# Kernel optimization log

Hardware: AMD Instinct MI355X
Metric: run time of the kernel (lower is better)

Reference implementation:

```python
import jax, jax.numpy as jnp
import numpy as np

EMBED_DIM = 1024
B, T = 8, 2048


def setup_inputs() -> dict:
    key = jax.random.key(0)
    kx, kw, kb = jax.random.split(key, 3)
    x = jax.random.normal(kx, (B, T, EMBED_DIM), dtype=jnp.float32)
    # nn.Linear(embed_dim, 3*embed_dim): weight [3E, E], bias [3E]
    bound = 1.0 / np.sqrt(EMBED_DIM)
    W = jax.random.uniform(kw, (3 * EMBED_DIM, EMBED_DIM), minval=-bound, maxval=bound, dtype=jnp.float32)
    b = jax.random.uniform(kb, (3 * EMBED_DIM,), minval=-bound, maxval=bound, dtype=jnp.float32)
    return {"x": x, "W": W, "b": b}


def reference(x, W, b):
    E = x.shape[-1]
    qkv = jnp.einsum('bte,fe->btf', x, W) + b            # [B,T,3E]
    q, k, v = jnp.split(qkv, 3, axis=-1)                 # each [B,T,E]
    scale = 1.0 / jnp.sqrt(jnp.asarray(E, dtype=x.dtype))
    scores = jnp.einsum('bqe,bke->bqk', q, k) * scale    # [B,T,T]
    Tq = x.shape[1]
    causal = jnp.tril(jnp.ones((Tq, Tq), dtype=bool))
    scores = jnp.where(causal[None, :, :], scores, jnp.asarray(-jnp.inf, dtype=x.dtype))
    attn = jax.nn.softmax(scores, axis=-1)
    y = jnp.einsum('bqk,bke->bqe', attn, v)              # [B,T,E]
    return y
```

## Files before the change

kernel.cpp:

```cpp
#include <hip/hip_runtime.h>

typedef unsigned short u16;
typedef unsigned int u32;
typedef __attribute__((ext_vector_type(4))) float f32x4;
typedef __attribute__((ext_vector_type(8))) short bf16x8;

#define T_DIM 2048
#define E_DIM 1024
#define NBATCH 8
#define BK 32
#define BUF 32768
#define CORE_LDS (3 * BUF)

struct alignas(8)  U16x4 { u16 x, y, z, w; };
struct alignas(16) F32x4 { float x, y, z, w; };

__device__ __forceinline__ u16 f2bf(float f) {
  u32 u = __float_as_uint(f);
  u += 0x7FFFu + ((u >> 16) & 1u);
  return (u16)(u >> 16);
}

__device__ __forceinline__ void gld16(u16* lds, const u16* g) {
  __builtin_amdgcn_global_load_lds((const __attribute__((address_space(1))) void*)g,
                                   (__attribute__((address_space(3))) void*)lds, 16, 0, 0);
}

__device__ __forceinline__ u32 swz7(u32 x) { return x ^ (((x >> 7) & 7u) << 4); }

__device__ __forceinline__ int xcd_swz(int orig, int nwg) {
  int q = nwg >> 3, r = nwg & 7;
  int x = orig & 7, l = orig >> 3;
  return (x < r ? x * (q + 1) : r * (q + 1) + (x - r) * q) + l;
}

#define LGKM0_PIN() do { asm volatile("s_waitcnt lgkmcnt(0)" ::: "memory"); \
                         __builtin_amdgcn_sched_barrier(0); } while (0)

template <typename HOOK>
__device__ __forceinline__ void gemm256(const u16* __restrict__ A, const u16* __restrict__ B,
                                        int lda, int ldb, int nK, char* lds0, f32x4 acc[8][4],
                                        HOOK&& hook)
{
  const int tid = threadIdx.x, lane = tid & 63, wave = tid >> 6;
  const int wr = wave >> 2, wc = wave & 3;

  const u16* sAp[2]; const u16* sBp[2];
#pragma unroll
  for (int c = 0; c < 2; ++c) {
    u32 L = (u32)(c * 8192 + tid * 16);
    u32 g = swz7(L);
    sAp[c] = A + (size_t)(g >> 6) * lda + ((g & 63u) >> 1);
    sBp[c] = B + (size_t)(g >> 6) * ldb + ((g & 63u) >> 1);
  }
  const u32 doff = (u32)tid * 16u;

  auto stageA = [&](char* buf, int t) {
#pragma unroll
    for (int c = 0; c < 2; ++c)
      gld16((u16*)(buf + c * 8192 + doff), sAp[c] + t * BK);
  };
  auto stageB = [&](char* buf, int t) {
#pragma unroll
    for (int c = 0; c < 2; ++c)
      gld16((u16*)(buf + 16384 + c * 8192 + doff), sBp[c] + t * BK);
  };

  const u32 cb = (u32)(lane >> 4) * 16u;
  u32 aoff[8], boff[4];
#pragma unroll
  for (int m = 0; m < 8; ++m)
    aoff[m] = swz7((u32)(wr * 128 + m * 16 + (lane & 15)) * 64u + cb);
#pragma unroll
  for (int n = 0; n < 4; ++n)
    boff[n] = 16384u + swz7((u32)(wc * 64 + n * 16 + (lane & 15)) * 64u + cb);

  stageA(lds0, 0); stageB(lds0, 0);
  stageA(lds0 + BUF, 1); stageB(lds0 + BUF, 1);

  int bc = 0;
  bf16x8 a[4], b[4];
  for (int t = 0; t < nK; ++t) {
    char* bufR = lds0 + bc * BUF;
    int b2 = bc + 2; if (b2 >= 3) b2 -= 3;
    char* bufW = lds0 + b2 * BUF;

    if (t + 1 < nK) asm volatile("s_waitcnt vmcnt(4)" ::: "memory");
    else            asm volatile("s_waitcnt vmcnt(0)" ::: "memory");
    __builtin_amdgcn_s_barrier();
    __builtin_amdgcn_sched_barrier(0);

    hook(t);

    if (t + 2 < nK) stageA(bufW, t + 2);
#pragma unroll
    for (int j = 0; j < 4; ++j) a[j] = *(const bf16x8*)(bufR + aoff[j]);
#pragma unroll
    for (int n = 0; n < 4; ++n) b[n] = *(const bf16x8*)(bufR + boff[n]);
    LGKM0_PIN();
    __builtin_amdgcn_s_setprio(1);
#pragma unroll
    for (int j = 0; j < 4; ++j)
#pragma unroll
      for (int n = 0; n < 4; ++n)
        acc[j][n] = __builtin_amdgcn_mfma_f32_16x16x32_bf16(a[j], b[n], acc[j][n], 0, 0, 0);
    __builtin_amdgcn_s_setprio(0);
    __builtin_amdgcn_sched_barrier(0);

    if (t + 2 < nK) stageB(bufW, t + 2);
#pragma unroll
    for (int j = 0; j < 4; ++j) a[j] = *(const bf16x8*)(bufR + aoff[4 + j]);
    LGKM0_PIN();
    __builtin_amdgcn_s_setprio(1);
#pragma unroll
    for (int j = 0; j < 4; ++j)
#pragma unroll
      for (int n = 0; n < 4; ++n)
        acc[4 + j][n] = __builtin_amdgcn_mfma_f32_16x16x32_bf16(a[j], b[n], acc[4 + j][n], 0, 0, 0);
    __builtin_amdgcn_s_setprio(0);
    __builtin_amdgcn_sched_barrier(0);

    bc = bc + 1 == 3 ? 0 : bc + 1;
  }
}

struct NoHook { __device__ void operator()(int) const {} };

__global__ __launch_bounds__(256) void k_cvt(const float* __restrict__ in, u16* __restrict__ out, int n4)
{
  int i = blockIdx.x * 256 + threadIdx.x;
  if (i >= n4) return;
  F32x4 v = *(const F32x4*)&in[(size_t)i * 4];
  U16x4 o;
  o.x = f2bf(v.x); o.y = f2bf(v.y); o.z = f2bf(v.z); o.w = f2bf(v.w);
  *(U16x4*)&out[(size_t)i * 4] = o;
}

__global__ __launch_bounds__(512, 2) void k_qkv(const u16* __restrict__ Xb, const u16* __restrict__ Wb,
                                                const float* __restrict__ bias,
                                                u16* __restrict__ Q, u16* __restrict__ Kmat,
                                                u16* __restrict__ Vt)
{
  __shared__ __align__(16) char lds[131072];
  const int wg = xcd_swz(blockIdx.x, gridDim.x);
  const int my = wg / 12, nx = wg % 12;
  const int m0 = my * 256, n0 = nx * 256;
  const int tid = threadIdx.x, lane = tid & 63, wave = tid >> 6;
  const int wr = wave >> 2, wc = wave & 3;
  f32x4 acc[8][4] = {};
  gemm256(Xb + (size_t)m0 * E_DIM, Wb + (size_t)n0 * E_DIM, E_DIM, E_DIM, E_DIM / BK,
          lds, acc, NoHook{});

  const int region = nx >> 2;
  if (region < 2) {
    u16* dst = region ? Kmat : Q;
#pragma unroll
    for (int n = 0; n < 4; ++n) {
      const int ng = n0 + wc * 64 + n * 16 + (lane & 15);
      const float bn = bias[ng];
      const int nl = ng & (E_DIM - 1);
#pragma unroll
      for (int m = 0; m < 8; ++m) {
        const int mg0 = m0 + wr * 128 + m * 16 + ((lane >> 4) << 2);
#pragma unroll
        for (int r = 0; r < 4; ++r)
          dst[(size_t)(mg0 + r) * E_DIM + nl] = f2bf(acc[m][n][r] + bn);
      }
    }
  } else {
    __syncthreads();
    char* wslice = lds + wave * 16384;
#pragma unroll
    for (int n = 0; n < 4; ++n) {
      const int ng = n0 + wc * 64 + n * 16 + (lane & 15);
      const float bn = bias[ng];
#pragma unroll
      for (int m = 0; m < 8; ++m) {
#pragma unroll
        for (int rp = 0; rp < 4; rp += 2) {
          u32 w = (u32)f2bf(acc[m][n][rp] + bn) | ((u32)f2bf(acc[m][n][rp + 1] + bn) << 16);
          u32 eb = (u32)((n * 16 + (lane & 15)) * 256 + (m * 16 + ((lane >> 4) << 2) + rp) * 2);
          eb ^= ((eb >> 8) & 7u) << 4;
          *(u32*)(wslice + eb) = w;
        }
      }
    }
    asm volatile("s_waitcnt lgkmcnt(0)" ::: "memory");
    const int bl = m0 >> 11;
    const int t_base = (m0 & (T_DIM - 1)) + wr * 128;
    const int nl_base = (n0 & (E_DIM - 1)) + wc * 64;
    const int t8 = (lane & 15) * 8;
#pragma unroll
    for (int k = 0; k < 16; ++k) {
      const int e_loc = (lane >> 4) + k * 4;
      u32 eb = (u32)(e_loc * 256 + t8 * 2);
      eb ^= ((eb >> 8) & 7u) << 4;
      bf16x8 v = *(const bf16x8*)(wslice + eb);
      *(bf16x8*)&Vt[((size_t)bl * E_DIM + nl_base + e_loc) * T_DIM + t_base + t8] = v;
    }
  }
}

__global__ __launch_bounds__(512, 2) void k_sp(const u16* __restrict__ Q, const u16* __restrict__ Kmat,
                                               u16* __restrict__ P, float* __restrict__ mc,
                                               float* __restrict__ lc)
{
  __shared__ __align__(16) char lds[CORE_LDS];
  const int wg = xcd_swz(blockIdx.x, gridDim.x);
  const int b = wg / 36;
  const int ti = wg % 36;
  int iq = 0;
  while ((iq + 1) * (iq + 2) / 2 <= ti) ++iq;
  const int ik = ti - iq * (iq + 1) / 2;
  const int tid = threadIdx.x, lane = tid & 63, wave = tid >> 6;
  const int wr = wave >> 2, wc = wave & 3;
  f32x4 acc[8][4] = {};
  const u16* Qp = Q    + (size_t)b * T_DIM * E_DIM + (size_t)iq * 256 * E_DIM;
  const u16* Kp = Kmat + (size_t)b * T_DIM * E_DIM + (size_t)ik * 256 * E_DIM;
  gemm256(Qp, Kp, E_DIM, E_DIM, E_DIM / BK, lds, acc, NoHook{});
  __syncthreads();

  const float scale = 0.03125f;
#pragma unroll
  for (int m = 0; m < 8; ++m)
#pragma unroll
    for (int n = 0; n < 4; ++n)
#pragma unroll
      for (int r = 0; r < 4; ++r) acc[m][n][r] *= scale;
  if (ik == iq) {
#pragma unroll
    for (int n = 0; n < 4; ++n) {
      const int kg = wc * 64 + n * 16 + (lane & 15);
#pragma unroll
      for (int m = 0; m < 8; ++m) {
        const int qg0 = wr * 128 + m * 16 + ((lane >> 4) << 2);
#pragma unroll
        for (int r = 0; r < 4; ++r)
          if (kg > qg0 + r) acc[m][n][r] = -3.4e38f;
      }
    }
  }

  float* red  = (float*)lds;
  float* red2 = (float*)lds + 1024;
  float M[8][4];
#pragma unroll
  for (int m = 0; m < 8; ++m)
#pragma unroll
    for (int r = 0; r < 4; ++r) {
      float v = fmaxf(fmaxf(acc[m][0][r], acc[m][1][r]), fmaxf(acc[m][2][r], acc[m][3][r]));
#pragma unroll
      for (int off = 1; off <= 8; off <<= 1) v = fmaxf(v, __shfl_xor(v, off, 64));
      M[m][r] = v;
    }
  if ((lane & 15) == 0) {
#pragma unroll
    for (int m = 0; m < 8; ++m)
#pragma unroll
      for (int r = 0; r < 4; ++r)
        red[wc * 256 + wr * 128 + m * 16 + ((lane >> 4) << 2) + r] = M[m][r];
  }
  __syncthreads();
#pragma unroll
  for (int m = 0; m < 8; ++m)
#pragma unroll
    for (int r = 0; r < 4; ++r) {
      const int row = wr * 128 + m * 16 + ((lane >> 4) << 2) + r;
      M[m][r] = fmaxf(fmaxf(red[row], red[256 + row]), fmaxf(red[512 + row], red[768 + row]));
    }

  u16* Pb = P + (size_t)b * T_DIM * T_DIM;
  float Ls[8][4];
#pragma unroll
  for (int m = 0; m < 8; ++m) {
    const int qg0 = iq * 256 + wr * 128 + m * 16 + ((lane >> 4) << 2);
#pragma unroll
    for (int r = 0; r < 4; ++r) {
      float s = 0.f;
      u16* prow = Pb + (size_t)(qg0 + r) * T_DIM + ik * 256;
#pragma unroll
      for (int n = 0; n < 4; ++n) {
        float e = __expf(acc[m][n][r] - M[m][r]);
        s += e;
        prow[wc * 64 + n * 16 + (lane & 15)] = f2bf(e);
      }
#pragma unroll
      for (int off = 1; off <= 8; off <<= 1) s += __shfl_xor(s, off, 64);
      Ls[m][r] = s;
    }
  }
  if ((lane & 15) == 0) {
#pragma unroll
    for (int m = 0; m < 8; ++m)
#pragma unroll
      for (int r = 0; r < 4; ++r)
        red2[wc * 256 + wr * 128 + m * 16 + ((lane >> 4) << 2) + r] = Ls[m][r];
  }
  __syncthreads();
  if (wc == 0 && (lane & 15) == 0) {
#pragma unroll
    for (int m = 0; m < 8; ++m)
#pragma unroll
      for (int r = 0; r < 4; ++r) {
        const int row = wr * 128 + m * 16 + ((lane >> 4) << 2) + r;
        const float l = red2[row] + red2[256 + row] + red2[512 + row] + red2[768 + row];
        const size_t idx = ((size_t)b * T_DIM + iq * 256 + row) * 8 + ik;
        mc[idx] = M[m][r];
        lc[idx] = l;
      }
  }
}

__global__ __launch_bounds__(256) void k_finish(const float* __restrict__ mc, const float* __restrict__ lc,
                                                float* __restrict__ fin)
{
  const int rg = blockIdx.x * 256 + threadIdx.x;
  const int q = rg & (T_DIM - 1);
  const int C = (q >> 8) + 1;
  const float* m = mc + (size_t)rg * 8;
  const float* l = lc + (size_t)rg * 8;
  float M = -3.4e38f;
  for (int c = 0; c < C; ++c) M = fmaxf(M, m[c]);
  float L = 0.f;
  for (int c = 0; c < C; ++c) L += l[c] * __expf(m[c] - M);
  fin[rg] = __expf(m[C - 1] - M) / L;
}

__global__ __launch_bounds__(512, 2) void k_pv(const u16* __restrict__ P, const u16* __restrict__ Vt,
                                               const float* __restrict__ mc, const float* __restrict__ fin,
                                               float* __restrict__ out, int batch0)
{
  __shared__ __align__(16) char lds[CORE_LDS + 8192];
  const int wg = xcd_swz(blockIdx.x, gridDim.x);
  const int bl = wg >> 5, rr = wg & 31;
  const int iq = rr >> 2, ie = rr & 3;
  const int tid = threadIdx.x, lane = tid & 63, wave = tid >> 6;
  const int wr = wave >> 2, wc = wave & 3;

  float* ldsM = (float*)(lds + CORE_LDS);
  const float* mrow = mc + ((size_t)bl * T_DIM + iq * 256) * 8;
  for (int i = tid; i < 2048; i += 512) ldsM[i] = mrow[i];
  asm volatile("s_waitcnt vmcnt(0) lgkmcnt(0)" ::: "memory");
  __builtin_amdgcn_s_barrier();

  f32x4 acc[8][4] = {};
  const u16* Ap = P  + (size_t)bl * T_DIM * T_DIM + (size_t)iq * 256 * T_DIM;
  const u16* Bp = Vt + (size_t)bl * E_DIM * T_DIM + (size_t)ie * 256 * T_DIM;

  auto rescale = [&](int t) {
    if (t > 0 && (t & 7) == 0) {
      const int c = t >> 3;
#pragma unroll
      for (int m = 0; m < 8; ++m)
#pragma unroll
        for (int r = 0; r < 4; ++r) {
          const int row = wr * 128 + m * 16 + ((lane >> 4) << 2) + r;
          const float mp = ldsM[row * 8 + (c - 1)];
          const float mn = ldsM[row * 8 + c];
          const float h = __expf(mp - mn);
#pragma unroll
          for (int n = 0; n < 4; ++n) acc[m][n][r] *= h;
        }
    }
  };
  gemm256(Ap, Bp, T_DIM, T_DIM, (iq + 1) * 8, lds, acc, rescale);

#pragma unroll
  for (int m = 0; m < 8; ++m) {
    const int qg0 = iq * 256 + wr * 128 + m * 16 + ((lane >> 4) << 2);
#pragma unroll
    for (int r = 0; r < 4; ++r) {
      const int qg = qg0 + r;
      const float il = fin[bl * T_DIM + qg];
      float* orow = out + ((size_t)(batch0 + bl) * T_DIM + qg) * E_DIM;
#pragma unroll
      for (int n = 0; n < 4; ++n) {
        const int eg = ie * 256 + wc * 64 + n * 16 + (lane & 15);
        orow[eg] = acc[m][n][r] * il;
      }
    }
  }
}

extern "C" void kernel_launch(void* const* d_in, const int* in_sizes, int n_in,
                              void* d_out, int out_size, void* d_ws, size_t ws_size,
                              hipStream_t stream)
{
  const float* x    = (const float*)d_in[0];
  const float* W    = (const float*)d_in[1];
  const float* bias = (const float*)d_in[2];
  float* out = (float*)d_out;

  char* ws = (char*)d_ws;
  const size_t ALIGN = 256;
  auto up = [&](size_t v) { return (v + ALIGN - 1) & ~(ALIGN - 1); };

  const size_t szWb = up((size_t)3 * E_DIM * E_DIM * 2);
  const size_t szX  = up((size_t)T_DIM * E_DIM * 2);
  const size_t szP  = up((size_t)T_DIM * T_DIM * 2);
  const size_t szM  = up((size_t)T_DIM * 8 * 4);
  const size_t szI  = up((size_t)T_DIM * 4);
  const size_t perB = 4 * szX + szP + 2 * szM + szI;

  int nb = 1;
  for (int cand = NBATCH; cand >= 1; --cand) {
    if (szWb + (size_t)cand * perB <= ws_size) { nb = cand; break; }
  }

  u16* Wb = (u16*)ws;
  {
    int n4 = 3 * E_DIM * E_DIM / 4;
    k_cvt<<<(n4 + 255) / 256, 256, 0, stream>>>(W, Wb, n4);
  }

  for (int b0 = 0; b0 < NBATCH; b0 += nb) {
    const int nbc = (NBATCH - b0 < nb) ? (NBATCH - b0) : nb;
    size_t o = szWb;
    u16* Xb    = (u16*)(ws + o);   o += (size_t)nbc * szX;
    u16* Qb    = (u16*)(ws + o);   o += (size_t)nbc * szX;
    u16* Kb    = (u16*)(ws + o);   o += (size_t)nbc * szX;
    u16* Vt    = (u16*)(ws + o);   o += (size_t)nbc * szX;
    u16* P     = (u16*)(ws + o);   o += (size_t)nbc * szP;
    float* mcA = (float*)(ws + o); o += (size_t)nbc * szM;
    float* lcA = (float*)(ws + o); o += (size_t)nbc * szM;
    float* fin = (float*)(ws + o); o += (size_t)nbc * szI;

    {
      int n4 = nbc * T_DIM * E_DIM / 4;
      k_cvt<<<(n4 + 255) / 256, 256, 0, stream>>>(x + (size_t)b0 * T_DIM * E_DIM, Xb, n4);
    }
    k_qkv<<<dim3(96 * nbc), 512, 0, stream>>>(Xb, Wb, bias, Qb, Kb, Vt);
    k_sp<<<dim3(36 * nbc), 512, 0, stream>>>(Qb, Kb, P, mcA, lcA);
    k_finish<<<dim3(nbc * T_DIM / 256), 256, 0, stream>>>(mcA, lcA, fin);
    k_pv<<<dim3(32 * nbc), 512, 0, stream>>>(P, Vt, mcA, fin, out, b0);
  }
}
```

Baseline: 272.6 us.

## Shrink GEMM tiles to 128x128 with simple single-buffered LDS loop

Replaces the 256x256, 512-thread, triple-buffered LDS pipeline with a 128x128, 256-thread GEMM that has a single LDS buffer and two barriers per K step, then re-tiles the QKV, score and PV kernels to match. The chunk statistics grow from 8 to 16 chunks per row, and Q/K stores now go through LDS for coalesced 16-byte writes. The smaller tiles give more workgroups and finer causal skipping, but they drop the async prefetch overlap and lower per-tile data reuse, so global traffic per FLOP rises.

```diff
diff --git a/kernel.cpp b/kernel.cpp
--- a/kernel.cpp
+++ b/kernel.cpp
@@ -9,8 +9,6 @@
 #define E_DIM 1024
 #define NBATCH 8
 #define BK 32
-#define BUF 32768
-#define CORE_LDS (3 * BUF)
 
 struct alignas(8)  U16x4 { u16 x, y, z, w; };
 struct alignas(16) F32x4 { float x, y, z, w; };
@@ -34,93 +32,52 @@
   return (x < r ? x * (q + 1) : r * (q + 1) + (x - r) * q) + l;
 }
 
-#define LGKM0_PIN() do { asm volatile("s_waitcnt lgkmcnt(0)" ::: "memory"); \
-                         __builtin_amdgcn_sched_barrier(0); } while (0)
-
 template <typename HOOK>
-__device__ __forceinline__ void gemm256(const u16* __restrict__ A, const u16* __restrict__ B,
-                                        int lda, int ldb, int nK, char* lds0, f32x4 acc[8][4],
+__device__ __forceinline__ void gemm128(const u16* __restrict__ A, const u16* __restrict__ B,
+                                        int lda, int ldb, int nK, char* lds0, f32x4 acc[4][4],
                                         HOOK&& hook)
 {
   const int tid = threadIdx.x, lane = tid & 63, wave = tid >> 6;
-  const int wr = wave >> 2, wc = wave & 3;
-
-  const u16* sAp[2]; const u16* sBp[2];
-#pragma unroll
-  for (int c = 0; c < 2; ++c) {
-    u32 L = (u32)(c * 8192 + tid * 16);
-    u32 g = swz7(L);
-    sAp[c] = A + (size_t)(g >> 6) * lda + ((g & 63u) >> 1);
-    sBp[c] = B + (size_t)(g >> 6) * ldb + ((g & 63u) >> 1);
+  const int wr = wave >> 1, wc = wave & 1;
+
+  const u16 *sA0, *sA1, *sB0, *sB1;
+  {
+    u32 L0 = (u32)tid * 16u, L1 = L0 + 4096u;
+    u32 g0 = swz7(L0), g1 = swz7(L1);
+    sA0 = A + (size_t)(g0 >> 6) * lda + ((g0 & 63u) >> 1);
+    sA1 = A + (size_t)(g1 >> 6) * lda + ((g1 & 63u) >> 1);
+    sB0 = B + (size_t)(g0 >> 6) * ldb + ((g0 & 63u) >> 1);
+    sB1 = B + (size_t)(g1 >> 6) * ldb + ((g1 & 63u) >> 1);
   }
   const u32 doff = (u32)tid * 16u;
 
-  auto stageA = [&](char* buf, int t) {
-#pragma unroll
-    for (int c = 0; c < 2; ++c)
-      gld16((u16*)(buf + c * 8192 + doff), sAp[c] + t * BK);
-  };
-  auto stageB = [&](char* buf, int t) {
-#pragma unroll
-    for (int c = 0; c < 2; ++c)
-      gld16((u16*)(buf + 16384 + c * 8192 + doff), sBp[c] + t * BK);
-  };
-
   const u32 cb = (u32)(lane >> 4) * 16u;
-  u32 aoff[8], boff[4];
-#pragma unroll
-  for (int m = 0; m < 8; ++m)
-    aoff[m] = swz7((u32)(wr * 128 + m * 16 + (lane & 15)) * 64u + cb);
+  u32 aoff[4], boff[4];
+#pragma unroll
+  for (int m = 0; m < 4; ++m)
+    aoff[m] = swz7((u32)(wr * 64 + m * 16 + (lane & 15)) * 64u + cb);
 #pragma unroll
   for (int n = 0; n < 4; ++n)
-    boff[n] = 16384u + swz7((u32)(wc * 64 + n * 16 + (lane & 15)) * 64u + cb);
-
-  stageA(lds0, 0); stageB(lds0, 0);
-  stageA(lds0 + BUF, 1); stageB(lds0 + BUF, 1);
-
-  int bc = 0;
-  bf16x8 a[4], b[4];
+    boff[n] = 8192u + swz7((u32)(wc * 64 + n * 16 + (lane & 15)) * 64u + cb);
+
   for (int t = 0; t < nK; ++t) {
-    char* bufR = lds0 + bc * BUF;
-    int b2 = bc + 2; if (b2 >= 3) b2 -= 3;
-    char* bufW = lds0 + b2 * BUF;
-
-    if (t + 1 < nK) asm volatile("s_waitcnt vmcnt(4)" ::: "memory");
-    else            asm volatile("s_waitcnt vmcnt(0)" ::: "memory");
-    __builtin_amdgcn_s_barrier();
-    __builtin_amdgcn_sched_barrier(0);
-
+    __syncthreads();
+    gld16((u16*)(lds0 + doff),         sA0 + t * BK);
+    gld16((u16*)(lds0 + 4096 + doff),  sA1 + t * BK);
+    gld16((u16*)(lds0 + 8192 + doff),  sB0 + t * BK);
+    gld16((u16*)(lds0 + 12288 + doff), sB1 + t * BK);
     hook(t);
-
-    if (t + 2 < nK) stageA(bufW, t + 2);
-#pragma unroll
-    for (int j = 0; j < 4; ++j) a[j] = *(const bf16x8*)(bufR + aoff[j]);
-#pragma unroll
-    for (int n = 0; n < 4; ++n) b[n] = *(const bf16x8*)(bufR + boff[n]);
-    LGKM0_PIN();
-    __builtin_amdgcn_s_setprio(1);
-#pragma unroll
-    for (int j = 0; j < 4; ++j)
+    __syncthreads();
+    bf16x8 a[4], b[4];
+#pragma unroll
+    for (int m = 0; m < 4; ++m) a[m] = *(const bf16x8*)(lds0 + aoff[m]);
+#pragma unroll
+    for (int n = 0; n < 4; ++n) b[n] = *(const bf16x8*)(lds0 + boff[n]);
+#pragma unroll
+    for (int m = 0; m < 4; ++m)
 #pragma unroll
       for (int n = 0; n < 4; ++n)
-        acc[j][n] = __builtin_amdgcn_mfma_f32_16x16x32_bf16(a[j], b[n], acc[j][n], 0, 0, 0);
-    __builtin_amdgcn_s_setprio(0);
-    __builtin_amdgcn_sched_barrier(0);
-
-    if (t + 2 < nK) stageB(bufW, t + 2);
-#pragma unroll
-    for (int j = 0; j < 4; ++j) a[j] = *(const bf16x8*)(bufR + aoff[4 + j]);
-    LGKM0_PIN();
-    __builtin_amdgcn_s_setprio(1);
-#pragma unroll
-    for (int j = 0; j < 4; ++j)
-#pragma unroll
-      for (int n = 0; n < 4; ++n)
-        acc[4 + j][n] = __builtin_amdgcn_mfma_f32_16x16x32_bf16(a[j], b[n], acc[4 + j][n], 0, 0, 0);
-    __builtin_amdgcn_s_setprio(0);
-    __builtin_amdgcn_sched_barrier(0);
-
-    bc = bc + 1 == 3 ? 0 : bc + 1;
+        acc[m][n] = __builtin_amdgcn_mfma_f32_16x16x32_bf16(a[m], b[n], acc[m][n], 0, 0, 0);
   }
 }
 
@@ -136,93 +93,102 @@
   *(U16x4*)&out[(size_t)i * 4] = o;
 }
 
-__global__ __launch_bounds__(512, 2) void k_qkv(const u16* __restrict__ Xb, const u16* __restrict__ Wb,
-                                                const float* __restrict__ bias,
-                                                u16* __restrict__ Q, u16* __restrict__ Kmat,
-                                                u16* __restrict__ Vt)
-{
-  __shared__ __align__(16) char lds[131072];
+__global__ __launch_bounds__(256) void k_qkv(const u16* __restrict__ Xb, const u16* __restrict__ Wb,
+                                             const float* __restrict__ bias,
+                                             u16* __restrict__ Q, u16* __restrict__ Kmat,
+                                             u16* __restrict__ Vt)
+{
+  __shared__ __align__(16) char lds[32768];
   const int wg = xcd_swz(blockIdx.x, gridDim.x);
-  const int my = wg / 12, nx = wg % 12;
-  const int m0 = my * 256, n0 = nx * 256;
+  const int my = wg / 24, nx = wg % 24;
+  const int m0 = my * 128, n0 = nx * 128;
   const int tid = threadIdx.x, lane = tid & 63, wave = tid >> 6;
-  const int wr = wave >> 2, wc = wave & 3;
-  f32x4 acc[8][4] = {};
-  gemm256(Xb + (size_t)m0 * E_DIM, Wb + (size_t)n0 * E_DIM, E_DIM, E_DIM, E_DIM / BK,
+  const int wr = wave >> 1, wc = wave & 1;
+  f32x4 acc[4][4] = {};
+  gemm128(Xb + (size_t)m0 * E_DIM, Wb + (size_t)n0 * E_DIM, E_DIM, E_DIM, E_DIM / BK,
           lds, acc, NoHook{});
-
-  const int region = nx >> 2;
+  __syncthreads();
+
+  char* wsl = lds + wave * 8192;
+  const int region = nx >> 3;
+
   if (region < 2) {
     u16* dst = region ? Kmat : Q;
 #pragma unroll
     for (int n = 0; n < 4; ++n) {
       const int ng = n0 + wc * 64 + n * 16 + (lane & 15);
       const float bn = bias[ng];
-      const int nl = ng & (E_DIM - 1);
-#pragma unroll
-      for (int m = 0; m < 8; ++m) {
-        const int mg0 = m0 + wr * 128 + m * 16 + ((lane >> 4) << 2);
-#pragma unroll
-        for (int r = 0; r < 4; ++r)
-          dst[(size_t)(mg0 + r) * E_DIM + nl] = f2bf(acc[m][n][r] + bn);
-      }
+#pragma unroll
+      for (int m = 0; m < 4; ++m)
+#pragma unroll
+        for (int r = 0; r < 4; ++r) {
+          const int row_l = m * 16 + ((lane >> 4) << 2) + r;
+          const int col_l = n * 16 + (lane & 15);
+          u32 byte = (u32)(row_l * 128 + col_l * 2) ^ (u32)((row_l & 7) << 4);
+          *(u16*)(wsl + byte) = f2bf(acc[m][n][r] + bn);
+        }
+    }
+    const int mgb = m0 + wr * 64;
+    const int nlb = (n0 & (E_DIM - 1)) + wc * 64;
+#pragma unroll
+    for (int it = 0; it < 8; ++it) {
+      const int row_l = it * 8 + (lane >> 3);
+      const int c16 = lane & 7;
+      u32 byte = (u32)(row_l * 128 + c16 * 16) ^ (u32)((row_l & 7) << 4);
+      bf16x8 v = *(const bf16x8*)(wsl + byte);
+      *(bf16x8*)&dst[(size_t)(mgb + row_l) * E_DIM + nlb + c16 * 8] = v;
     }
   } else {
-    __syncthreads();
-    char* wslice = lds + wave * 16384;
 #pragma unroll
     for (int n = 0; n < 4; ++n) {
       const int ng = n0 + wc * 64 + n * 16 + (lane & 15);
       const float bn = bias[ng];
-#pragma unroll
-      for (int m = 0; m < 8; ++m) {
-#pragma unroll
-        for (int rp = 0; rp < 4; rp += 2) {
-          u32 w = (u32)f2bf(acc[m][n][rp] + bn) | ((u32)f2bf(acc[m][n][rp + 1] + bn) << 16);
-          u32 eb = (u32)((n * 16 + (lane & 15)) * 256 + (m * 16 + ((lane >> 4) << 2) + rp) * 2);
-          eb ^= ((eb >> 8) & 7u) << 4;
-          *(u32*)(wslice + eb) = w;
+      const int e_l = n * 16 + (lane & 15);
+#pragma unroll
+      for (int m = 0; m < 4; ++m)
+#pragma unroll
+        for (int r = 0; r < 4; ++r) {
+          const int t_l = m * 16 + ((lane >> 4) << 2) + r;
+          u32 byte = (u32)(e_l * 128 + t_l * 2) ^ (u32)((e_l & 7) << 4);
+          *(u16*)(wsl + byte) = f2bf(acc[m][n][r] + bn);
         }
-      }
-    }
-    asm volatile("s_waitcnt lgkmcnt(0)" ::: "memory");
+    }
     const int bl = m0 >> 11;
-    const int t_base = (m0 & (T_DIM - 1)) + wr * 128;
-    const int nl_base = (n0 & (E_DIM - 1)) + wc * 64;
-    const int t8 = (lane & 15) * 8;
-#pragma unroll
-    for (int k = 0; k < 16; ++k) {
-      const int e_loc = (lane >> 4) + k * 4;
-      u32 eb = (u32)(e_loc * 256 + t8 * 2);
-      eb ^= ((eb >> 8) & 7u) << 4;
-      bf16x8 v = *(const bf16x8*)(wslice + eb);
-      *(bf16x8*)&Vt[((size_t)bl * E_DIM + nl_base + e_loc) * T_DIM + t_base + t8] = v;
-    }
-  }
-}
-
-__global__ __launch_bounds__(512, 2) void k_sp(const u16* __restrict__ Q, const u16* __restrict__ Kmat,
-                                               u16* __restrict__ P, float* __restrict__ mc,
-                                               float* __restrict__ lc)
-{
-  __shared__ __align__(16) char lds[CORE_LDS];
+    const int tb = (m0 & (T_DIM - 1)) + wr * 64;
+    const int nlb = (n0 & (E_DIM - 1)) + wc * 64;
+#pragma unroll
+    for (int it = 0; it < 8; ++it) {
+      const int e_l = it * 8 + (lane >> 3);
+      const int t16 = lane & 7;
+      u32 byte = (u32)(e_l * 128 + t16 * 16) ^ (u32)((e_l & 7) << 4);
+      bf16x8 v = *(const bf16x8*)(wsl + byte);
+      *(bf16x8*)&Vt[((size_t)bl * E_DIM + nlb + e_l) * T_DIM + tb + t16 * 8] = v;
+    }
+  }
+}
+
+__global__ __launch_bounds__(256) void k_sp(const u16* __restrict__ Q, const u16* __restrict__ Kmat,
+                                            u16* __restrict__ P, float* __restrict__ mc,
+                                            float* __restrict__ lc)
+{
+  __shared__ __align__(16) char lds[16384];
   const int wg = xcd_swz(blockIdx.x, gridDim.x);
-  const int b = wg / 36;
-  const int ti = wg % 36;
+  const int b = wg / 136;
+  const int ti = wg % 136;
   int iq = 0;
   while ((iq + 1) * (iq + 2) / 2 <= ti) ++iq;
   const int ik = ti - iq * (iq + 1) / 2;
   const int tid = threadIdx.x, lane = tid & 63, wave = tid >> 6;
-  const int wr = wave >> 2, wc = wave & 3;
-  f32x4 acc[8][4] = {};
-  const u16* Qp = Q    + (size_t)b * T_DIM * E_DIM + (size_t)iq * 256 * E_DIM;
-  const u16* Kp = Kmat + (size_t)b * T_DIM * E_DIM + (size_t)ik * 256 * E_DIM;
-  gemm256(Qp, Kp, E_DIM, E_DIM, E_DIM / BK, lds, acc, NoHook{});
+  const int wr = wave >> 1, wc = wave & 1;
+  f32x4 acc[4][4] = {};
+  const u16* Qp = Q    + (size_t)b * T_DIM * E_DIM + (size_t)iq * 128 * E_DIM;
+  const u16* Kp = Kmat + (size_t)b * T_DIM * E_DIM + (size_t)ik * 128 * E_DIM;
+  gemm128(Qp, Kp, E_DIM, E_DIM, E_DIM / BK, lds, acc, NoHook{});
   __syncthreads();
 
   const float scale = 0.03125f;
 #pragma unroll
-  for (int m = 0; m < 8; ++m)
+  for (int m = 0; m < 4; ++m)
 #pragma unroll
     for (int n = 0; n < 4; ++n)
 #pragma unroll
@@ -232,8 +198,8 @@
     for (int n = 0; n < 4; ++n) {
       const int kg = wc * 64 + n * 16 + (lane & 15);
 #pragma unroll
-      for (int m = 0; m < 8; ++m) {
-        const int qg0 = wr * 128 + m * 16 + ((lane >> 4) << 2);
+      for (int m = 0; m < 4; ++m) {
+        const int qg0 = wr * 64 + m * 16 + ((lane >> 4) << 2);
 #pragma unroll
         for (int r = 0; r < 4; ++r)
           if (kg > qg0 + r) acc[m][n][r] = -3.4e38f;
@@ -242,10 +208,10 @@
   }
 
   float* red  = (float*)lds;
-  float* red2 = (float*)lds + 1024;
-  float M[8][4];
-#pragma unroll
-  for (int m = 0; m < 8; ++m)
+  float* red2 = red + 256;
+  float M[4][4];
+#pragma unroll
+  for (int m = 0; m < 4; ++m)
 #pragma unroll
     for (int r = 0; r < 4; ++r) {
       float v = fmaxf(fmaxf(acc[m][0][r], acc[m][1][r]), fmaxf(acc[m][2][r], acc[m][3][r]));
@@ -255,29 +221,29 @@
     }
   if ((lane & 15) == 0) {
 #pragma unroll
-    for (int m = 0; m < 8; ++m)
+    for (int m = 0; m < 4; ++m)
 #pragma unroll
       for (int r = 0; r < 4; ++r)
-        red[wc * 256 + wr * 128 + m * 16 + ((lane >> 4) << 2) + r] = M[m][r];
+        red[wc * 128 + wr * 64 + m * 16 + ((lane >> 4) << 2) + r] = M[m][r];
   }
   __syncthreads();
 #pragma unroll
-  for (int m = 0; m < 8; ++m)
+  for (int m = 0; m < 4; ++m)
 #pragma unroll
     for (int r = 0; r < 4; ++r) {
-      const int row = wr * 128 + m * 16 + ((lane >> 4) << 2) + r;
-      M[m][r] = fmaxf(fmaxf(red[row], red[256 + row]), fmaxf(red[512 + row], red[768 + row]));
+      const int row = wr * 64 + m * 16 + ((lane >> 4) << 2) + r;
+      M[m][r] = fmaxf(red[row], red[128 + row]);
     }
 
   u16* Pb = P + (size_t)b * T_DIM * T_DIM;
-  float Ls[8][4];
-#pragma unroll
-  for (int m = 0; m < 8; ++m) {
-    const int qg0 = iq * 256 + wr * 128 + m * 16 + ((lane >> 4) << 2);
+  float Ls[4][4];
+#pragma unroll
+  for (int m = 0; m < 4; ++m) {
+    const int qg0 = iq * 128 + wr * 64 + m * 16 + ((lane >> 4) << 2);
 #pragma unroll
     for (int r = 0; r < 4; ++r) {
       float s = 0.f;
-      u16* prow = Pb + (size_t)(qg0 + r) * T_DIM + ik * 256;
+      u16* prow = Pb + (size_t)(qg0 + r) * T_DIM + ik * 128;
 #pragma unroll
       for (int n = 0; n < 4; ++n) {
         float e = __expf(acc[m][n][r] - M[m][r]);
@@ -291,20 +257,20 @@
   }
   if ((lane & 15) == 0) {
 #pragma unroll
-    for (int m = 0; m < 8; ++m)
+    for (int m = 0; m < 4; ++m)
 #pragma unroll
       for (int r = 0; r < 4; ++r)
-        red2[wc * 256 + wr * 128 + m * 16 + ((lane >> 4) << 2) + r] = Ls[m][r];
+        red2[wc * 128 + wr * 64 + m * 16 + ((lane >> 4) << 2) + r] = Ls[m][r];
   }
   __syncthreads();
   if (wc == 0 && (lane & 15) == 0) {
 #pragma unroll
-    for (int m = 0; m < 8; ++m)
+    for (int m = 0; m < 4; ++m)
 #pragma unroll
       for (int r = 0; r < 4; ++r) {
-        const int row = wr * 128 + m * 16 + ((lane >> 4) << 2) + r;
-        const float l = red2[row] + red2[256 + row] + red2[512 + row] + red2[768 + row];
-        const size_t idx = ((size_t)b * T_DIM + iq * 256 + row) * 8 + ik;
+        const int row = wr * 64 + m * 16 + ((lane >> 4) << 2) + r;
+        const float l = red2[row] + red2[128 + row];
+        const size_t idx = ((size_t)b * T_DIM + iq * 128 + row) * 16 + ik;
         mc[idx] = M[m][r];
         lc[idx] = l;
       }
@@ -316,9 +282,9 @@
 {
   const int rg = blockIdx.x * 256 + threadIdx.x;
   const int q = rg & (T_DIM - 1);
-  const int C = (q >> 8) + 1;
-  const float* m = mc + (size_t)rg * 8;
-  const float* l = lc + (size_t)rg * 8;
+  const int C = (q >> 7) + 1;
+  const float* m = mc + (size_t)rg * 16;
+  const float* l = lc + (size_t)rg * 16;
   float M = -3.4e38f;
   for (int c = 0; c < C; ++c) M = fmaxf(M, m[c]);
   float L = 0.f;
@@ -326,48 +292,45 @@
   fin[rg] = __expf(m[C - 1] - M) / L;
 }
 
-__global__ __launch_bounds__(512, 2) void k_pv(const u16* __restrict__ P, const u16* __restrict__ Vt,
-                                               const float* __restrict__ mc, const float* __restrict__ fin,
-                                               float* __restrict__ out, int batch0)
-{
-  __shared__ __align__(16) char lds[CORE_LDS + 8192];
+__global__ __launch_bounds__(256) void k_pv(const u16* __restrict__ P, const u16* __restrict__ Vt,
+                                            const float* __restrict__ mc, const float* __restrict__ fin,
+                                            float* __restrict__ out, int batch0)
+{
+  __shared__ __align__(16) char lds[24576];
   const int wg = xcd_swz(blockIdx.x, gridDim.x);
-  const int bl = wg >> 5, rr = wg & 31;
-  const int iq = rr >> 2, ie = rr & 3;
+  const int bl = wg >> 7, rr = wg & 127;
+  const int iq = rr >> 3, ie = rr & 7;
   const int tid = threadIdx.x, lane = tid & 63, wave = tid >> 6;
-  const int wr = wave >> 2, wc = wave & 3;
-
-  float* ldsM = (float*)(lds + CORE_LDS);
-  const float* mrow = mc + ((size_t)bl * T_DIM + iq * 256) * 8;
-  for (int i = tid; i < 2048; i += 512) ldsM[i] = mrow[i];
-  asm volatile("s_waitcnt vmcnt(0) lgkmcnt(0)" ::: "memory");
-  __builtin_amdgcn_s_barrier();
-
-  f32x4 acc[8][4] = {};
-  const u16* Ap = P  + (size_t)bl * T_DIM * T_DIM + (size_t)iq * 256 * T_DIM;
-  const u16* Bp = Vt + (size_t)bl * E_DIM * T_DIM + (size_t)ie * 256 * T_DIM;
+  const int wr = wave >> 1, wc = wave & 1;
+
+  float* ldsM = (float*)(lds + 16384);
+  const float* mrow = mc + ((size_t)bl * T_DIM + iq * 128) * 16;
+  for (int i = tid; i < 2048; i += 256) ldsM[i] = mrow[i];
+  __syncthreads();
+
+  f32x4 acc[4][4] = {};
+  const u16* Ap = P  + (size_t)bl * T_DIM * T_DIM + (size_t)iq * 128 * T_DIM;
+  const u16* Bp = Vt + (size_t)bl * E_DIM * T_DIM + (size_t)ie * 128 * T_DIM;
 
   auto rescale = [&](int t) {
-    if (t > 0 && (t & 7) == 0) {
-      const int c = t >> 3;
-#pragma unroll
-      for (int m = 0; m < 8; ++m)
+    if (t > 0 && (t & 3) == 0) {
+      const int c = t >> 2;
+#pragma unroll
+      for (int m = 0; m < 4; ++m)
 #pragma unroll
         for (int r = 0; r < 4; ++r) {
-          const int row = wr * 128 + m * 16 + ((lane >> 4) << 2) + r;
-          const float mp = ldsM[row * 8 + (c - 1)];
-          const float mn = ldsM[row * 8 + c];
-          const float h = __expf(mp - mn);
+          const int row = wr * 64 + m * 16 + ((lane >> 4) << 2) + r;
+          const float h = __expf(ldsM[row * 16 + (c - 1)] - ldsM[row * 16 + c]);
 #pragma unroll
           for (int n = 0; n < 4; ++n) acc[m][n][r] *= h;
         }
     }
   };
-  gemm256(Ap, Bp, T_DIM, T_DIM, (iq + 1) * 8, lds, acc, rescale);
-
-#pragma unroll
-  for (int m = 0; m < 8; ++m) {
-    const int qg0 = iq * 256 + wr * 128 + m * 16 + ((lane >> 4) << 2);
+  gemm128(Ap, Bp, T_DIM, T_DIM, (iq + 1) * 4, lds, acc, rescale);
+
+#pragma unroll
+  for (int m = 0; m < 4; ++m) {
+    const int qg0 = iq * 128 + wr * 64 + m * 16 + ((lane >> 4) << 2);
 #pragma unroll
     for (int r = 0; r < 4; ++r) {
       const int qg = qg0 + r;
@@ -375,7 +338,7 @@
       float* orow = out + ((size_t)(batch0 + bl) * T_DIM + qg) * E_DIM;
 #pragma unroll
       for (int n = 0; n < 4; ++n) {
-        const int eg = ie * 256 + wc * 64 + n * 16 + (lane & 15);
+        const int eg = ie * 128 + wc * 64 + n * 16 + (lane & 15);
         orow[eg] = acc[m][n][r] * il;
       }
     }
@@ -398,7 +361,7 @@
   const size_t szWb = up((size_t)3 * E_DIM * E_DIM * 2);
   const size_t szX  = up((size_t)T_DIM * E_DIM * 2);
   const size_t szP  = up((size_t)T_DIM * T_DIM * 2);
-  const size_t szM  = up((size_t)T_DIM * 8 * 4);
+  const size_t szM  = up((size_t)T_DIM * 16 * 4);
   const size_t szI  = up((size_t)T_DIM * 4);
   const size_t perB = 4 * szX + szP + 2 * szM + szI;
 
@@ -429,9 +392,9 @@
       int n4 = nbc * T_DIM * E_DIM / 4;
       k_cvt<<<(n4 + 255) / 256, 256, 0, stream>>>(x + (size_t)b0 * T_DIM * E_DIM, Xb, n4);
     }
-    k_qkv<<<dim3(96 * nbc), 512, 0, stream>>>(Xb, Wb, bias, Qb, Kb, Vt);
-    k_sp<<<dim3(36 * nbc), 512, 0, stream>>>(Qb, Kb, P, mcA, lcA);
+    k_qkv<<<dim3(24 * 16 * nbc), 256, 0, stream>>>(Xb, Wb, bias, Qb, Kb, Vt);
+    k_sp<<<dim3(136 * nbc), 256, 0, stream>>>(Qb, Kb, P, mcA, lcA);
     k_finish<<<dim3(nbc * T_DIM / 256), 256, 0, stream>>>(mcA, lcA, fin);
-    k_pv<<<dim3(32 * nbc), 512, 0, stream>>>(P, Vt, mcA, fin, out, b0);
-  }
-}
+    k_pv<<<dim3(128 * nbc), 256, 0, stream>>>(P, Vt, mcA, fin, out, b0);
+  }
+}
```

New measurement: 301.1 us. 10.5% more time.
